# Kernel tuning notes

Hardware: AMD Instinct MI355X
Metric: run time of the kernel (lower is better)

## Reference

```python
import jax, jax.numpy as jnp
import numpy as np

TEMPERATURE = 0.07
C_MARGIN = 0.5
T_MARGIN = 1.0
GAMMA = 2.0
ALPHA = 0.25
SMOOTHING = 0.1
W_CONTRASTIVE = 0.1
W_TRIPLET = 0.1
W_FOCAL = 0.4
W_LABEL_SMOOTH = 0.4


def setup_inputs() -> dict:
    key = jax.random.key(0)
    k1, k2, k3 = jax.random.split(key, 3)
    B, C, D = 2048, 1000, 512
    pred = jax.random.normal(k1, (B, C), dtype=jnp.float32)
    target = jax.random.randint(k2, (B,), 0, C, dtype=jnp.int64)
    features = jax.random.normal(k3, (B, D), dtype=jnp.float32)
    return {"pred": pred, "target": target, "features": features}


def _safe_cdist(f):
    # Euclidean pairwise distance with zero-grad at zero distance (matches torch.cdist on diagonal).
    r = jnp.sum(f * f, axis=1)
    d2 = jnp.maximum(r[:, None] - 2.0 * (f @ f.T) + r[None, :], 0.0)
    pos = d2 > 0
    return jnp.sqrt(jnp.where(pos, d2, 1.0)) * pos


def _contrastive(features, labels):
    f = features / jnp.linalg.norm(features, axis=1, keepdims=True)
    sim = f @ f.T  # [B, B]
    lm = (labels[:, None] == labels[None, :]).astype(sim.dtype)
    pos = sim * lm
    pos_loss = -jnp.log(jnp.exp(pos / TEMPERATURE) + 1e-8)
    neg = sim * (1.0 - lm)
    neg_loss = jnp.maximum(C_MARGIN - neg, 0.0)
    return pos_loss.mean() + neg_loss.mean()


def _triplet(features, labels):
    B = features.shape[0]
    d = _safe_cdist(features)  # [B, B]
    lm = (labels[:, None] == labels[None, :]).astype(d.dtype)
    pm, nm = lm, 1.0 - lm

    def body(acc, args):
        di, pmi, nmi = args  # [B], [B], [B]
        # sum over (p, n): relu(d_ip - d_in + margin), masked
        contrib = jnp.sum(
            jnp.maximum(di[:, None] - di[None, :] + T_MARGIN, 0.0)
            * pmi[:, None] * nmi[None, :]
        )
        return acc + contrib, None

    loss, _ = jax.lax.scan(body, jnp.float32(0.0), (d, pm, nm))
    return loss / (B + 1e-8)


def _focal(pred, target):
    logp = jax.nn.log_softmax(pred, axis=1)
    ce = -jnp.take_along_axis(logp, target[:, None], axis=1)[:, 0]
    pt = jnp.exp(-ce)
    return (ALPHA * (1.0 - pt) ** GAMMA * ce).mean()


def _label_smoothing(pred, target):
    C = pred.shape[1]
    off = SMOOTHING / (C - 1)
    logp = jax.nn.log_softmax(pred, axis=1)
    # smooth target: off everywhere, (1 - smoothing) at target index
    tgt_logp = jnp.take_along_axis(logp, target[:, None], axis=1)[:, 0]
    loss = -(off * logp.sum(axis=1) + ((1.0 - SMOOTHING) - off) * tgt_logp)
    return loss.mean()


def reference(pred, target, features):
    lc = _contrastive(features, target)
    lt = _triplet(features, target)
    lf = _focal(pred, target)
    ls = _label_smoothing(pred, target)
    total = (W_CONTRASTIVE * lc + W_TRIPLET * lt
             + W_FOCAL * lf + W_LABEL_SMOOTH * ls)
    return jnp.stack([lc, lt, lf, ls, total])
```

## Files before the change

kernel.cpp:

```cpp
#include <hip/hip_runtime.h>
#include <hip/hip_bf16.h>
#include <math.h>

typedef __attribute__((ext_vector_type(8))) short bf16x8;
typedef __attribute__((ext_vector_type(4))) float f32x4;

static constexpr float TEMP_INV  = 1.0f / 0.07f;
static constexpr float C_MARGIN  = 0.5f;
static constexpr float T_MARGIN  = 1.0f;
static constexpr float ALPHA     = 0.25f;
static constexpr float SMOOTHING = 0.1f;

__device__ __forceinline__ void gload_lds16(const void* g, void* l) {
    __builtin_amdgcn_global_load_lds(
        (const __attribute__((address_space(1))) void*)g,
        (__attribute__((address_space(3))) void*)l,
        16, 0, 0);
}

__device__ __forceinline__ unsigned short f2bf(float x) {
    __hip_bfloat16 h = __float2bfloat16(x);
    return *reinterpret_cast<unsigned short*>(&h);
}
__device__ __forceinline__ float bf2f(unsigned short u) {
    union { unsigned int u32; float f; } U;
    U.u32 = ((unsigned int)u) << 16;
    return U.f;
}

__global__ __launch_bounds__(256) void prep_kernel(
    const float* __restrict__ F, unsigned short* __restrict__ Fb,
    float* __restrict__ diag, float* __restrict__ inv_norm, int D) {
    const int row  = blockIdx.x * 4 + (threadIdx.x >> 6);
    const int lane = threadIdx.x & 63;
    const float4* Fr  = (const float4*)(F + (size_t)row * D);
    ushort4*      Fbr = (ushort4*)(Fb + (size_t)row * D);
    const int n4 = D >> 2;
    float s = 0.0f;
    for (int idx = lane; idx < n4; idx += 64) {
        float4 v = Fr[idx];
        s += v.x * v.x + v.y * v.y + v.z * v.z + v.w * v.w;
        ushort4 o;
        o.x = f2bf(v.x); o.y = f2bf(v.y); o.z = f2bf(v.z); o.w = f2bf(v.w);
        Fbr[idx] = o;
    }
#pragma unroll
    for (int off = 32; off > 0; off >>= 1) s += __shfl_down(s, off, 64);
    if (lane == 0) { diag[row] = s; inv_norm[row] = 1.0f / sqrtf(s); }
}

__global__ __launch_bounds__(256) void gram_ce_kernel(
    const unsigned short* __restrict__ Fb, unsigned short* __restrict__ Gb,
    const float* __restrict__ pred, const int* __restrict__ target,
    float* __restrict__ partialCE, int B, int D, int C, float off_const,
    int tilesX) {
    __shared__ unsigned short As[128 * 64];
    __shared__ unsigned short Bs[128 * 64];
    __shared__ float red[12];

    const int nTiles = tilesX * tilesX;
    const int tid = threadIdx.x;
    const int lane = tid & 63, wid = tid >> 6;

    if (blockIdx.x < nTiles) {
        const int rowBase = (blockIdx.x / tilesX) * 128;
        const int colBase = (blockIdx.x % tilesX) * 128;
        const int w = wid, l = lane;
        const int wr = (w >> 1) * 64;
        const int wc = (w & 1) * 64;
        const int half = l >> 4;
        const int rr   = l & 15;

        const unsigned short* FA = Fb + (size_t)rowBase * D;
        const unsigned short* FB = Fb + (size_t)colBase * D;

        f32x4 acc[4][4];
#pragma unroll
        for (int m = 0; m < 4; ++m)
#pragma unroll
            for (int n = 0; n < 4; ++n) acc[m][n] = (f32x4){0.f, 0.f, 0.f, 0.f};

        for (int k0 = 0; k0 < D; k0 += 64) {
#pragma unroll
            for (int c = 0; c < 4; ++c) {
                const int chunk = c * 256 + w * 64 + l;
                const int r2 = chunk >> 3;
                const int ss = (l & 7) ^ (r2 & 7);
                const size_t eoff = (size_t)r2 * D + k0 + ss * 8;
                gload_lds16(FA + eoff, &As[(c * 256 + w * 64) * 8]);
                gload_lds16(FB + eoff, &Bs[(c * 256 + w * 64) * 8]);
            }
            __syncthreads();
#pragma unroll
            for (int kk2 = 0; kk2 < 2; ++kk2) {
                const int s = kk2 * 4 + half;
                bf16x8 af[4], bfv[4];
#pragma unroll
                for (int f = 0; f < 4; ++f) {
                    const int ar = wr + f * 16 + rr;
                    af[f]  = *(const bf16x8*)(&As[ar * 64 + ((s ^ (ar & 7)) * 8)]);
                    const int br = wc + f * 16 + rr;
                    bfv[f] = *(const bf16x8*)(&Bs[br * 64 + ((s ^ (br & 7)) * 8)]);
                }
#pragma unroll
                for (int m = 0; m < 4; ++m)
#pragma unroll
                    for (int n = 0; n < 4; ++n)
                        acc[m][n] = __builtin_amdgcn_mfma_f32_16x16x32_bf16(
                            af[m], bfv[n], acc[m][n], 0, 0, 0);
            }
            __syncthreads();
        }
#pragma unroll
        for (int m = 0; m < 4; ++m) {
            const int i0 = rowBase + wr + m * 16 + half * 4;
#pragma unroll
            for (int n = 0; n < 4; ++n) {
                const int j = colBase + wc + n * 16 + rr;
#pragma unroll
                for (int r = 0; r < 4; ++r)
                    Gb[(size_t)(i0 + r) * B + j] = f2bf(acc[m][n][r]);
            }
        }
    } else {
        const int i = blockIdx.x - nTiles;
        const float* prow = pred + (size_t)i * C;
        const float tlogit = prow[target[i]];
        const int Cv = C >> 2;

        float m = -1e30f, s = 0.0f, sp = 0.0f;
        for (int idx = tid; idx < Cv; idx += 256) {
            float4 v = ((const float4*)prow)[idx];
            float mv = fmaxf(fmaxf(v.x, v.y), fmaxf(v.z, v.w));
            if (mv > m) { s *= expf(m - mv); m = mv; }
            s += expf(v.x - m) + expf(v.y - m) + expf(v.z - m) + expf(v.w - m);
            sp += v.x + v.y + v.z + v.w;
        }
        for (int j = Cv * 4 + tid; j < C; j += 256) {
            float v = prow[j];
            if (v > m) { s *= expf(m - v); m = v; }
            s += expf(v - m);
            sp += v;
        }
#pragma unroll
        for (int off = 32; off > 0; off >>= 1) {
            float mo = __shfl_down(m, off, 64);
            float so = __shfl_down(s, off, 64);
            sp += __shfl_down(sp, off, 64);
            float mx = fmaxf(m, mo);
            s = s * expf(m - mx) + so * expf(mo - mx);
            m = mx;
        }
        if (lane == 0) { red[wid] = m; red[4 + wid] = s; red[8 + wid] = sp; }
        __syncthreads();
        if (tid == 0) {
            float mm = red[0], ss = red[4], spT = red[8];
#pragma unroll
            for (int q = 1; q < 4; ++q) {
                float mo = red[q], so = red[4 + q];
                float mn = fmaxf(mm, mo);
                ss = ss * expf(mm - mn) + so * expf(mo - mn);
                mm = mn;
                spT += red[8 + q];
            }
            float lse = mm + logf(ss);
            float tl  = tlogit - lse;
            float ce  = -tl;
            float pt  = expf(tl);
            float omp = 1.0f - pt;
            float focal = ALPHA * omp * omp * ce;
            float sumlogp = spT - (float)C * lse;
            float lsv = -(off_const * sumlogp + ((1.0f - SMOOTHING) - off_const) * tl);
            partialCE[(size_t)i * 2]     = focal;
            partialCE[(size_t)i * 2 + 1] = lsv;
        }
    }
}

__global__ __launch_bounds__(256) void row_loss_kernel(
    const unsigned short* __restrict__ Gb, const float* __restrict__ diag,
    const float* __restrict__ inv_norm, const int* __restrict__ labels,
    float* __restrict__ partial, int B) {
    __shared__ float p_d[256];
    __shared__ float red[12];
    __shared__ int p_cnt;
    const int tid = threadIdx.x;
    const int i = blockIdx.x;
    if (tid == 0) p_cnt = 0;
    __syncthreads();

    const int   li     = labels[i];
    const float ri     = diag[i];
    const float inv_ni = inv_norm[i];
    const int   j0     = tid * 8;

    union { uint4 u; unsigned short s[8]; } GV;
    GV.u = *(const uint4*)(Gb + (size_t)i * B + j0);
    int lab[8];
    *(int4*)&lab[0] = *(const int4*)(labels + j0);
    *(int4*)&lab[4] = *(const int4*)(labels + j0 + 4);
    float dg[8], ivn[8];
    *(float4*)&dg[0]  = *(const float4*)(diag + j0);
    *(float4*)&dg[4]  = *(const float4*)(diag + j0 + 4);
    *(float4*)&ivn[0] = *(const float4*)(inv_norm + j0);
    *(float4*)&ivn[4] = *(const float4*)(inv_norm + j0 + 4);

    float pos = 0.0f, neg = 0.0f;
    float d8[8];
    int mmask = 0;
#pragma unroll
    for (int e = 0; e < 8; ++e) {
        const int j = j0 + e;
        const float g = bf2f(GV.s[e]);
        float sim = g * inv_ni * ivn[e];
        const float d2 = ri - 2.0f * g + dg[e];
        float d = (d2 > 0.0f) ? sqrtf(d2) : 0.0f;
        if (j == i) { sim = 1.0f; d = 0.0f; }
        d8[e] = d;
        if (lab[e] == li) {
            pos += -logf(expf(sim * TEMP_INV) + 1e-8f);
            neg += C_MARGIN;
            mmask |= (1 << e);
            int slot = atomicAdd(&p_cnt, 1);
            if (slot < 256) p_d[slot] = d;
        } else {
            neg += fmaxf(C_MARGIN - sim, 0.0f);
        }
    }
    __syncthreads();
    const int cnt = (p_cnt < 256) ? p_cnt : 256;
    float trip = 0.0f;
    for (int p = 0; p < cnt; ++p) {
        const float dp = p_d[p] + T_MARGIN;
#pragma unroll
        for (int e = 0; e < 8; ++e)
            if (!(mmask & (1 << e))) trip += fmaxf(dp - d8[e], 0.0f);
    }

    float r0 = pos, r1 = neg, r2 = trip;
#pragma unroll
    for (int off = 32; off > 0; off >>= 1) {
        r0 += __shfl_down(r0, off, 64);
        r1 += __shfl_down(r1, off, 64);
        r2 += __shfl_down(r2, off, 64);
    }
    const int lane = tid & 63, wid = tid >> 6;
    if (lane == 0) { red[wid] = r0; red[4 + wid] = r1; red[8 + wid] = r2; }
    __syncthreads();
    if (tid == 0) {
        float4 o;
        o.x = red[0] + red[1] + red[2] + red[3];
        o.y = red[4] + red[5] + red[6] + red[7];
        o.z = red[8] + red[9] + red[10] + red[11];
        o.w = 0.0f;
        *(float4*)(partial + (size_t)i * 4) = o;
    }
}

__global__ __launch_bounds__(256) void reduce_kernel(
    const float* __restrict__ partialT, const float* __restrict__ partialCE,
    float* __restrict__ out, int B) {
    __shared__ float red[4][5];
    const int tid = threadIdx.x;
    float s[5] = {0.f, 0.f, 0.f, 0.f, 0.f};
    for (int r = tid; r < B; r += 256) {
        float4 v = *(const float4*)(partialT + (size_t)r * 4);
        s[0] += v.x; s[1] += v.y; s[2] += v.z;
    }
    for (int t = tid; t < (B * 2) / 4; t += 256) {
        float4 v = *(const float4*)(partialCE + (size_t)t * 4);
        s[3] += v.x + v.z; s[4] += v.y + v.w;
    }
#pragma unroll
    for (int off = 32; off > 0; off >>= 1) {
#pragma unroll
        for (int k = 0; k < 5; ++k) s[k] += __shfl_down(s[k], off, 64);
    }
    const int lane = tid & 63, wid = tid >> 6;
    if (lane == 0) {
#pragma unroll
        for (int k = 0; k < 5; ++k) red[wid][k] = s[k];
    }
    __syncthreads();
    if (tid == 0) {
        float t[5];
#pragma unroll
        for (int k = 0; k < 5; ++k)
            t[k] = red[0][k] + red[1][k] + red[2][k] + red[3][k];
        double invB2 = 1.0 / ((double)B * (double)B);
        float lc = (float)(((double)t[0] + (double)t[1]) * invB2);
        float lt = (float)((double)t[2] / ((double)B + 1e-8));
        float lf = t[3] / (float)B;
        float ls = t[4] / (float)B;
        out[0] = lc;
        out[1] = lt;
        out[2] = lf;
        out[3] = ls;
        out[4] = 0.1f * lc + 0.1f * lt + 0.4f * lf + 0.4f * ls;
    }
}

extern "C" void kernel_launch(void* const* d_in, const int* in_sizes, int n_in,
                              void* d_out, int out_size, void* d_ws, size_t ws_size,
                              hipStream_t stream) {
    const float* pred     = (const float*)d_in[0];
    const int*   target   = (const int*)d_in[1];
    const float* features = (const float*)d_in[2];
    const int B = in_sizes[1];
    const int C = in_sizes[0] / B;
    const int D = in_sizes[2] / B;
    float* out = (float*)d_out;
    const int tilesX = B / 128;
    const int nTiles = tilesX * tilesX;

    float* partial   = (float*)d_ws;
    float* partialCE = partial + (size_t)B * 4;
    float* diag      = partialCE + (size_t)B * 2;
    float* inv_norm  = diag + B;
    unsigned short* Fb = (unsigned short*)(inv_norm + B);
    unsigned short* Gb = Fb + (size_t)B * D;

    prep_kernel<<<B / 4, 256, 0, stream>>>(features, Fb, diag, inv_norm, D);

    float off_const = SMOOTHING / (float)(C - 1);
    gram_ce_kernel<<<nTiles + B, 256, 0, stream>>>(
        Fb, Gb, pred, target, partialCE, B, D, C, off_const, tilesX);

    row_loss_kernel<<<B, 256, 0, stream>>>(Gb, diag, inv_norm, target,
                                           partial, B);

    reduce_kernel<<<1, 256, 0, stream>>>(partial, partialCE, out, B);
}
```

Measured before the change: 38.02 us.

## Fuse bf16 feature conversion and norm computation into gram/CE kernel

Removes the separate prep kernel. The gram tiles now load fp32 features straight into LDS, with k-steps of 32, and convert them to bf16 in registers before the MFMA. Row squared norms and inverse norms are now computed in the CE blocks of the same kernel. This drops one launch and the bf16 staging buffer. In exchange, the gram tiles read twice as many global bytes, convert redundantly in every tile, and take more k-iterations with a barrier each.

Result: no change. 37.85 us (-0.4%).

```diff
diff --git a/kernel.cpp b/kernel.cpp
--- a/kernel.cpp
+++ b/kernel.cpp
@@ -27,36 +27,25 @@
     U.u32 = ((unsigned int)u) << 16;
     return U.f;
 }
-
-__global__ __launch_bounds__(256) void prep_kernel(
-    const float* __restrict__ F, unsigned short* __restrict__ Fb,
-    float* __restrict__ diag, float* __restrict__ inv_norm, int D) {
-    const int row  = blockIdx.x * 4 + (threadIdx.x >> 6);
-    const int lane = threadIdx.x & 63;
-    const float4* Fr  = (const float4*)(F + (size_t)row * D);
-    ushort4*      Fbr = (ushort4*)(Fb + (size_t)row * D);
-    const int n4 = D >> 2;
-    float s = 0.0f;
-    for (int idx = lane; idx < n4; idx += 64) {
-        float4 v = Fr[idx];
-        s += v.x * v.x + v.y * v.y + v.z * v.z + v.w * v.w;
-        ushort4 o;
-        o.x = f2bf(v.x); o.y = f2bf(v.y); o.z = f2bf(v.z); o.w = f2bf(v.w);
-        Fbr[idx] = o;
-    }
-#pragma unroll
-    for (int off = 32; off > 0; off >>= 1) s += __shfl_down(s, off, 64);
-    if (lane == 0) { diag[row] = s; inv_norm[row] = 1.0f / sqrtf(s); }
+__device__ __forceinline__ bf16x8 pack8(float4 a, float4 b) {
+    bf16x8 r;
+    r[0] = (short)f2bf(a.x); r[1] = (short)f2bf(a.y);
+    r[2] = (short)f2bf(a.z); r[3] = (short)f2bf(a.w);
+    r[4] = (short)f2bf(b.x); r[5] = (short)f2bf(b.y);
+    r[6] = (short)f2bf(b.z); r[7] = (short)f2bf(b.w);
+    return r;
 }
 
 __global__ __launch_bounds__(256) void gram_ce_kernel(
-    const unsigned short* __restrict__ Fb, unsigned short* __restrict__ Gb,
+    const float* __restrict__ F, unsigned short* __restrict__ Gb,
     const float* __restrict__ pred, const int* __restrict__ target,
-    float* __restrict__ partialCE, int B, int D, int C, float off_const,
+    float* __restrict__ partialCE, float* __restrict__ diag,
+    float* __restrict__ inv_norm, int B, int D, int C, float off_const,
     int tilesX) {
-    __shared__ unsigned short As[128 * 64];
-    __shared__ unsigned short Bs[128 * 64];
+    __shared__ float Asf[128 * 32];
+    __shared__ float Bsf[128 * 32];
     __shared__ float red[12];
+    __shared__ float redn[4];
 
     const int nTiles = tilesX * tilesX;
     const int tid = threadIdx.x;
@@ -71,8 +60,8 @@
         const int half = l >> 4;
         const int rr   = l & 15;
 
-        const unsigned short* FA = Fb + (size_t)rowBase * D;
-        const unsigned short* FB = Fb + (size_t)colBase * D;
+        const float* FA = F + (size_t)rowBase * D;
+        const float* FB = F + (size_t)colBase * D;
 
         f32x4 acc[4][4];
 #pragma unroll
@@ -80,35 +69,37 @@
 #pragma unroll
             for (int n = 0; n < 4; ++n) acc[m][n] = (f32x4){0.f, 0.f, 0.f, 0.f};
 
-        for (int k0 = 0; k0 < D; k0 += 64) {
+        for (int k0 = 0; k0 < D; k0 += 32) {
 #pragma unroll
             for (int c = 0; c < 4; ++c) {
                 const int chunk = c * 256 + w * 64 + l;
                 const int r2 = chunk >> 3;
                 const int ss = (l & 7) ^ (r2 & 7);
-                const size_t eoff = (size_t)r2 * D + k0 + ss * 8;
-                gload_lds16(FA + eoff, &As[(c * 256 + w * 64) * 8]);
-                gload_lds16(FB + eoff, &Bs[(c * 256 + w * 64) * 8]);
+                const size_t eoff = (size_t)r2 * D + k0 + ss * 4;
+                gload_lds16(FA + eoff, &Asf[(c * 256 + w * 64) * 4]);
+                gload_lds16(FB + eoff, &Bsf[(c * 256 + w * 64) * 4]);
             }
             __syncthreads();
-#pragma unroll
-            for (int kk2 = 0; kk2 < 2; ++kk2) {
-                const int s = kk2 * 4 + half;
-                bf16x8 af[4], bfv[4];
-#pragma unroll
-                for (int f = 0; f < 4; ++f) {
-                    const int ar = wr + f * 16 + rr;
-                    af[f]  = *(const bf16x8*)(&As[ar * 64 + ((s ^ (ar & 7)) * 8)]);
-                    const int br = wc + f * 16 + rr;
-                    bfv[f] = *(const bf16x8*)(&Bs[br * 64 + ((s ^ (br & 7)) * 8)]);
-                }
-#pragma unroll
-                for (int m = 0; m < 4; ++m)
-#pragma unroll
-                    for (int n = 0; n < 4; ++n)
-                        acc[m][n] = __builtin_amdgcn_mfma_f32_16x16x32_bf16(
-                            af[m], bfv[n], acc[m][n], 0, 0, 0);
+            bf16x8 af[4], bfv[4];
+#pragma unroll
+            for (int f = 0; f < 4; ++f) {
+                const int ar = wr + f * 16 + rr;
+                const float* rp = &Asf[ar * 32];
+                af[f] = pack8(
+                    *(const float4*)(rp + (((half * 2)     ^ (ar & 7)) * 4)),
+                    *(const float4*)(rp + (((half * 2 + 1) ^ (ar & 7)) * 4)));
+                const int br = wc + f * 16 + rr;
+                const float* cp = &Bsf[br * 32];
+                bfv[f] = pack8(
+                    *(const float4*)(cp + (((half * 2)     ^ (br & 7)) * 4)),
+                    *(const float4*)(cp + (((half * 2 + 1) ^ (br & 7)) * 4)));
             }
+#pragma unroll
+            for (int m = 0; m < 4; ++m)
+#pragma unroll
+                for (int n = 0; n < 4; ++n)
+                    acc[m][n] = __builtin_amdgcn_mfma_f32_16x16x32_bf16(
+                        af[m], bfv[n], acc[m][n], 0, 0, 0);
             __syncthreads();
         }
 #pragma unroll
@@ -124,10 +115,15 @@
         }
     } else {
         const int i = blockIdx.x - nTiles;
+        const float2* Fr2 = (const float2*)(F + (size_t)i * D);
+        float ns = 0.0f;
+        for (int idx = tid; idx < (D >> 1); idx += 256) {
+            float2 f = Fr2[idx];
+            ns += f.x * f.x + f.y * f.y;
+        }
         const float* prow = pred + (size_t)i * C;
         const float tlogit = prow[target[i]];
         const int Cv = C >> 2;
-
         float m = -1e30f, s = 0.0f, sp = 0.0f;
         for (int idx = tid; idx < Cv; idx += 256) {
             float4 v = ((const float4*)prow)[idx];
@@ -147,11 +143,14 @@
             float mo = __shfl_down(m, off, 64);
             float so = __shfl_down(s, off, 64);
             sp += __shfl_down(sp, off, 64);
+            ns += __shfl_down(ns, off, 64);
             float mx = fmaxf(m, mo);
             s = s * expf(m - mx) + so * expf(mo - mx);
             m = mx;
         }
-        if (lane == 0) { red[wid] = m; red[4 + wid] = s; red[8 + wid] = sp; }
+        if (lane == 0) {
+            red[wid] = m; red[4 + wid] = s; red[8 + wid] = sp; redn[wid] = ns;
+        }
         __syncthreads();
         if (tid == 0) {
             float mm = red[0], ss = red[4], spT = red[8];
@@ -173,6 +172,9 @@
             float lsv = -(off_const * sumlogp + ((1.0f - SMOOTHING) - off_const) * tl);
             partialCE[(size_t)i * 2]     = focal;
             partialCE[(size_t)i * 2 + 1] = lsv;
+            float nst = redn[0] + redn[1] + redn[2] + redn[3];
+            diag[i] = nst;
+            inv_norm[i] = 1.0f / sqrtf(nst);
         }
     }
 }
@@ -317,14 +319,12 @@
     float* partialCE = partial + (size_t)B * 4;
     float* diag      = partialCE + (size_t)B * 2;
     float* inv_norm  = diag + B;
-    unsigned short* Fb = (unsigned short*)(inv_norm + B);
-    unsigned short* Gb = Fb + (size_t)B * D;
-
-    prep_kernel<<<B / 4, 256, 0, stream>>>(features, Fb, diag, inv_norm, D);
+    unsigned short* Gb = (unsigned short*)(inv_norm + B);
 
     float off_const = SMOOTHING / (float)(C - 1);
     gram_ce_kernel<<<nTiles + B, 256, 0, stream>>>(
-        Fb, Gb, pred, target, partialCE, B, D, C, off_const, tilesX);
+        features, Gb, pred, target, partialCE, diag, inv_norm,
+        B, D, C, off_const, tilesX);
 
     row_loss_kernel<<<B, 256, 0, stream>>>(Gb, diag, inv_norm, target,
                                            partial, B);
```
